# Performance work log

Measured on AMD Instinct MI355X. Metric: run time of the kernel, lower is better.

Reference implementation:

```python
import jax, jax.numpy as jnp
import numpy as np

B, S, EMB, HID, IMG, ATT, K, HL = 64, 512, 768, 512, 2048, 512, 6, 20


def setup_inputs() -> dict:
    key = jax.random.key(0)
    ks = jax.random.split(key, 14)
    u = lambda k, shape: jax.random.uniform(k, shape, jnp.float32, -0.1, 0.1)
    return {
        "representations": jax.random.normal(ks[0], (B, S, EMB), jnp.float32),
        "lengths": jax.random.randint(ks[1], (B,), 0, S),
        "separate_images": jax.random.normal(ks[2], (B, K, IMG), jnp.float32),
        "visual_context": jax.random.normal(ks[3], (B, K * IMG), jnp.float32),
        "prev_hist": jax.random.normal(ks[4], (B, K, HL, EMB), jnp.float32),
        "hist_counts": jax.random.randint(ks[5], (B, K), 0, HL + 1),
        "masks": jax.random.randint(ks[6], (B, S, 1), 0, 2).astype(bool),
        "W_sep": u(ks[7], (IMG, HID)), "b_sep": jnp.zeros((HID,), jnp.float32),
        "W_e2h": u(ks[8], (EMB, HID)), "b_e2h": jnp.zeros((HID,), jnp.float32),
        "W_hist": u(ks[9], (EMB, HID)), "b_hist": jnp.zeros((HID,), jnp.float32),
        "W_ctx": u(ks[10], (K * IMG, HID)), "b_ctx": jnp.zeros((HID,), jnp.float32),
        "W_mm": u(ks[11], (2 * HID, HID)), "b_mm": jnp.zeros((HID,), jnp.float32),
        "W_a1": u(ks[12], (HID, ATT)), "b_a1": jnp.zeros((ATT,), jnp.float32),
        "W_a2": u(ks[13], (ATT, 1)), "b_a2": jnp.zeros((1,), jnp.float32),
    }


def reference(representations, lengths, separate_images, visual_context,
              prev_hist, hist_counts, masks,
              W_sep, b_sep, W_e2h, b_e2h, W_hist, b_hist, W_ctx, b_ctx,
              W_mm, b_mm, W_a1, b_a1, W_a2, b_a2):
    # dropout_prob = 0 -> dropout is identity (eval-mode equivalence)
    input_reps = jax.nn.relu(representations @ W_e2h + b_e2h)          # [B,S,H]
    ctx = jax.nn.relu(visual_context @ W_ctx + b_ctx)                  # [B,H]
    ctx_rep = jnp.broadcast_to(ctx[:, None, :], input_reps.shape)
    mm = jax.nn.relu(jnp.concatenate([input_reps, ctx_rep], -1) @ W_mm + b_mm)  # [B,S,H]
    scores = jnp.tanh(mm @ W_a1 + b_a1) @ W_a2 + b_a2                  # [B,S,1]
    scores = jnp.where(masks, -jnp.inf, scores)
    att_w = jax.nn.softmax(scores, axis=1)                             # softmax over seq
    attended = jnp.sum(mm * att_w, axis=1)                             # [B,H]

    sep = separate_images @ W_sep + b_sep                              # [B,K,H]
    hl = prev_hist.shape[2]
    valid = jnp.arange(hl)[None, None, :] < hist_counts[:, :, None]    # [B,K,HL]
    hsum = jnp.sum(prev_hist * valid[..., None].astype(prev_hist.dtype), axis=2)
    havg = hsum / jnp.maximum(hist_counts, 1)[..., None].astype(prev_hist.dtype)
    hproj = jax.nn.relu(havg @ W_hist + b_hist)                        # [B,K,H]
    sep = sep + jnp.where((hist_counts > 0)[..., None], hproj, 0.0)
    sep = jax.nn.relu(sep)
    # F.normalize(p=2, dim=2, eps=1e-12)
    sep = sep / jnp.maximum(jnp.linalg.norm(sep, axis=2, keepdims=True), 1e-12)
    dot = jnp.einsum('bkh,bh->bk', sep, attended)[..., None]           # [B,K,1]
    return dot
```

## Files before the change

kernel.cpp:

```cpp
#include <hip/hip_runtime.h>
#include <math.h>

#define B_    64
#define S_    512
#define EMB_  768
#define HID_  512
#define IMG_  2048
#define ATT_  512
#define K_    6
#define HL_   20
#define MS_   (B_ * S_)

typedef __attribute__((ext_vector_type(8))) short bf16x8;
typedef __attribute__((ext_vector_type(4))) float f32x4;

__device__ __forceinline__ unsigned short f2b(float f) {
    unsigned int u = __float_as_uint(f);
    u += 0x7fffu + ((u >> 16) & 1u);
    return (unsigned short)(u >> 16);
}
__device__ __forceinline__ unsigned int pk_bf16(float lo, float hi) {
    unsigned int r;
    asm volatile("v_cvt_pk_bf16_f32 %0, %1, %2" : "=v"(r) : "v"(lo), "v"(hi));
    return r;
}

#define GLD_LDS16(gp, lp)                                                        \
    __builtin_amdgcn_global_load_lds(                                            \
        (const __attribute__((address_space(1))) void*)(gp),                     \
        (__attribute__((address_space(3))) void*)(lp), 16, 0, 0)

__global__ __launch_bounds__(256)
void prep(const float* __restrict__ W_e2h, const float* __restrict__ W_mm,
          const float* __restrict__ W_a1,
          unsigned short* __restrict__ WtE2H, unsigned short* __restrict__ WtMM,
          unsigned short* __restrict__ WtA1,
          const unsigned char* __restrict__ masks, int* __restrict__ flag) {
    const int z = blockIdx.z;
    if (z == 3) {
        if (blockIdx.x != 0 || blockIdx.y != 0) return;
        __shared__ int found;
        if (threadIdx.x == 0) found = 0;
        __syncthreads();
        for (int i = threadIdx.x; i < 8192; i += 256)
            if ((i & 3) != 0 && masks[i] != 0) found = 1;
        __syncthreads();
        if (threadIdx.x == 0) *flag = found;
        return;
    }
    const float* W;
    unsigned short* Wt;
    int Kd;
    if (z == 0)      { W = W_e2h; Wt = WtE2H; Kd = EMB_; }
    else if (z == 1) { W = W_mm;  Wt = WtMM;  Kd = HID_; }
    else             { W = W_a1;  Wt = WtA1;  Kd = HID_; }
    if ((int)blockIdx.x * 32 >= Kd) return;

    __shared__ float tile[32][33];
    int k0 = blockIdx.x * 32, n0 = blockIdx.y * 32;
    int tx = threadIdx.x & 31, ty = threadIdx.x >> 5;
    #pragma unroll
    for (int i = 0; i < 4; ++i)
        tile[ty + i * 8][tx] = W[(size_t)(k0 + ty + i * 8) * HID_ + n0 + tx];
    __syncthreads();
    #pragma unroll
    for (int i = 0; i < 4; ++i)
        Wt[(size_t)(n0 + ty + i * 8) * Kd + k0 + tx] = f2b(tile[tx][ty + i * 8]);
}

__device__ __forceinline__ void tile_coords(int N, int& bm, int& bn) {
    const int nwg = gridDim.x;
    const int cpx = nwg >> 3;
    const int lid = ((int)blockIdx.x & 7) * cpx + ((int)blockIdx.x >> 3);
    const int ntl = N >> 7;
    bn = (lid % ntl) << 7;
    bm = (lid / ntl) << 7;
}

template<bool AF32, int ACT, bool SCORE>
__global__ __launch_bounds__(256)
void gemm_bdir(const void* __restrict__ Av, const unsigned short* __restrict__ Bt,
               const float* __restrict__ bias, const float* __restrict__ row_add,
               int row_div, unsigned short* __restrict__ Co,
               const float* __restrict__ W_a2, float* __restrict__ scores8,
               int M, int N, int Kd) {
    __shared__ unsigned short Als[2][128 * 64];
    const int tid = threadIdx.x;
    int bm, bn; tile_coords(N, bm, bn);
    const int lane = tid & 63, wid = tid >> 6;
    const int wr = wid >> 1, wc = wid & 1;
    const int fr = lane & 15, hi = lane >> 4;

    const unsigned short* Ab = (const unsigned short*)Av;
    const float* Af = (const float*)Av;

    f32x4 acc[4][4] = {};

    int srow[4], lcol[4], scol[4];
    #pragma unroll
    for (int c = 0; c < 4; ++c) {
        int g = c * 256 + tid;
        srow[c] = g >> 3;
        lcol[c] = g & 7;
        scol[c] = lcol[c] ^ (srow[c] & 7);
    }

    const unsigned short* pB[4];
    #pragma unroll
    for (int n = 0; n < 4; ++n)
        pB[n] = Bt + (size_t)(bn + wc * 64 + n * 16 + fr) * Kd + hi * 8;

    float4 ra[8];

    auto stageA_lds = [&](int t, int buf) {
        #pragma unroll
        for (int c = 0; c < 4; ++c) {
            int g = c * 256 + tid;
            GLD_LDS16(Ab + (size_t)(bm + srow[c]) * Kd + t * 64 + scol[c] * 8,
                      &Als[buf][g * 8]);
        }
    };
    auto loadA = [&](int t) {
        #pragma unroll
        for (int c = 0; c < 4; ++c) {
            const float* p = Af + (size_t)(bm + srow[c]) * Kd + t * 64 + scol[c] * 8;
            ra[2 * c]     = *(const float4*)p;
            ra[2 * c + 1] = *(const float4*)(p + 4);
        }
    };
    auto writeA = [&](int buf) {
        #pragma unroll
        for (int c = 0; c < 4; ++c) {
            int g = c * 256 + tid;
            uint4 u;
            u.x = pk_bf16(ra[2*c].x,   ra[2*c].y);
            u.y = pk_bf16(ra[2*c].z,   ra[2*c].w);
            u.z = pk_bf16(ra[2*c+1].x, ra[2*c+1].y);
            u.w = pk_bf16(ra[2*c+1].z, ra[2*c+1].w);
            *(uint4*)&Als[buf][g * 8] = u;
        }
    };
    auto compute = [&](int buf, int t) {
        #pragma unroll
        for (int kk = 0; kk < 2; ++kk) {
            bf16x8 af[4], bv[4];
            #pragma unroll
            for (int n = 0; n < 4; ++n)
                bv[n] = *(const bf16x8*)(pB[n] + t * 64 + kk * 32);
            #pragma unroll
            for (int m = 0; m < 4; ++m) {
                int r = wr * 64 + m * 16 + fr;
                int sc = (kk * 4 + hi) ^ (fr & 7);
                af[m] = *(const bf16x8*)&Als[buf][r * 64 + sc * 8];
            }
            #pragma unroll
            for (int m = 0; m < 4; ++m)
                #pragma unroll
                for (int n = 0; n < 4; ++n)
                    acc[m][n] = __builtin_amdgcn_mfma_f32_16x16x32_bf16(af[m], bv[n], acc[m][n], 0, 0, 0);
        }
    };

    const int nt = Kd >> 6;

    if constexpr (AF32) {
        loadA(0);
        writeA(0);
    } else {
        stageA_lds(0, 0);
    }
    __syncthreads();

    for (int t = 0; t < nt; ++t) {
        const int buf = t & 1;
        const bool pf = (t + 1 < nt);
        if (pf) {
            if constexpr (AF32) loadA(t + 1);
            else                stageA_lds(t + 1, buf ^ 1);
        }
        compute(buf, t);
        if constexpr (AF32) {
            if (pf) writeA(buf ^ 1);
        }
        __syncthreads();
    }

    if (SCORE) {
        float ba[4], wa[4];
        #pragma unroll
        for (int n = 0; n < 4; ++n) {
            int col = bn + wc * 64 + n * 16 + fr;
            ba[n] = bias[col];
            wa[n] = W_a2[col];
        }
        const int slot = (bn >> 7) * 2 + wc;
        #pragma unroll
        for (int m = 0; m < 4; ++m) {
            #pragma unroll
            for (int r = 0; r < 4; ++r) {
                float p = 0.f;
                #pragma unroll
                for (int n = 0; n < 4; ++n)
                    p += tanhf(acc[m][n][r] + ba[n]) * wa[n];
                p += __shfl_xor(p, 1, 64);
                p += __shfl_xor(p, 2, 64);
                p += __shfl_xor(p, 4, 64);
                p += __shfl_xor(p, 8, 64);
                if (fr == 0)
                    scores8[(size_t)slot * M + bm + wr * 64 + m * 16 + hi * 4 + r] = p;
            }
        }
    } else {
        #pragma unroll
        for (int m = 0; m < 4; ++m) {
            #pragma unroll
            for (int n = 0; n < 4; ++n) {
                int col = bn + wc * 64 + n * 16 + fr;
                float badd = bias ? bias[col] : 0.f;
                #pragma unroll
                for (int r = 0; r < 4; ++r) {
                    int row = bm + wr * 64 + m * 16 + hi * 4 + r;
                    float x = acc[m][n][r] + badd;
                    if (row_add) x += row_add[(size_t)(row / row_div) * N + col];
                    if (ACT == 1) x = fmaxf(x, 0.f);
                    Co[(size_t)row * N + col] = f2b(x);
                }
            }
        }
    }
}

__global__ __launch_bounds__(256)
void gemm_splitk(const float* __restrict__ A, const float* __restrict__ W,
                 float* __restrict__ P, int M, int N, int Kd, int kps) {
    __shared__ float As[16][68];
    __shared__ float Ws[16][64];
    const int tid = threadIdx.x;
    const int bm = blockIdx.y * 64, bn = blockIdx.x * 64;
    const int ks = blockIdx.z;
    const int tx = tid & 15, ty = tid >> 4;
    const int arow = tid >> 2, akq = tid & 3;
    const int wk = tid >> 4, wnq = tid & 15;

    float acc[4][4] = {};
    const int kbeg = ks * kps, kend = kbeg + kps;

    for (int k0 = kbeg; k0 < kend; k0 += 16) {
        float4 av = *(const float4*)&A[(size_t)(bm + arow) * Kd + k0 + akq * 4];
        float4 wv = *(const float4*)&W[(size_t)(k0 + wk) * N + bn + wnq * 4];
        As[akq * 4 + 0][arow] = av.x;
        As[akq * 4 + 1][arow] = av.y;
        As[akq * 4 + 2][arow] = av.z;
        As[akq * 4 + 3][arow] = av.w;
        *(float4*)&Ws[wk][wnq * 4] = wv;
        __syncthreads();
        #pragma unroll
        for (int kk = 0; kk < 16; ++kk) {
            float4 a4 = *(const float4*)&As[kk][ty * 4];
            float4 b4 = *(const float4*)&Ws[kk][tx * 4];
            float a_[4] = {a4.x, a4.y, a4.z, a4.w};
            float b_[4] = {b4.x, b4.y, b4.z, b4.w};
            #pragma unroll
            for (int i = 0; i < 4; ++i)
                #pragma unroll
                for (int j = 0; j < 4; ++j)
                    acc[i][j] += a_[i] * b_[j];
        }
        __syncthreads();
    }

    float* Pbase = P + (size_t)ks * M * N;
    #pragma unroll
    for (int i = 0; i < 4; ++i) {
        int row = bm + ty * 4 + i;
        float4 v = {acc[i][0], acc[i][1], acc[i][2], acc[i][3]};
        *(float4*)&Pbase[(size_t)row * N + bn + tx * 4] = v;
    }
}

template<int ACT>
__global__ __launch_bounds__(256)
void reduce_k(const float* __restrict__ P, const float* __restrict__ bias,
              float* __restrict__ C, int MN, int N, int nsplit) {
    int idx = blockIdx.x * 256 + threadIdx.x;
    if (idx >= MN) return;
    float s = 0.f;
    for (int z = 0; z < nsplit; ++z) s += P[(size_t)z * MN + idx];
    if (bias) s += bias[idx & (N - 1)];
    if (ACT == 1) s = fmaxf(s, 0.f);
    C[idx] = s;
}

__global__ __launch_bounds__(256)
void softmax8(const float* __restrict__ scores8, const float* __restrict__ b_a2,
              const void* __restrict__ masks_raw, const int* __restrict__ flag,
              float* __restrict__ attw) {
    int b = blockIdx.x, tid = threadIdx.x;
    bool isb = (*flag) != 0;
    const unsigned char* mb = (const unsigned char*)masks_raw;
    const int* mi = (const int*)masks_raw;
    int lane = tid & 63, wv = tid >> 6;
    __shared__ float red[4], red2[4];
    float bias = b_a2[0];

    float m = -INFINITY;
    for (int s = tid; s < S_; s += 256) {
        int idx = b * S_ + s;
        float v = bias;
        #pragma unroll
        for (int z = 0; z < 8; ++z) v += scores8[(size_t)z * MS_ + idx];
        bool mk = isb ? (mb[idx] != 0) : (mi[idx] != 0);
        v = mk ? -INFINITY : v;
        attw[idx] = v;
        m = fmaxf(m, v);
    }
    #pragma unroll
    for (int off = 32; off; off >>= 1) m = fmaxf(m, __shfl_down(m, off, 64));
    if (lane == 0) red[wv] = m;
    __syncthreads();
    if (tid == 0) red[0] = fmaxf(fmaxf(red[0], red[1]), fmaxf(red[2], red[3]));
    __syncthreads();
    float Mx = red[0];

    float sum = 0.f;
    for (int s = tid; s < S_; s += 256) {
        int idx = b * S_ + s;
        float e = expf(attw[idx] - Mx);
        attw[idx] = e;
        sum += e;
    }
    #pragma unroll
    for (int off = 32; off; off >>= 1) sum += __shfl_down(sum, off, 64);
    if (lane == 0) red2[wv] = sum;
    __syncthreads();
    if (tid == 0) red2[0] = red2[0] + red2[1] + red2[2] + red2[3];
    __syncthreads();
    float inv = 1.f / red2[0];
    for (int s = tid; s < S_; s += 256) attw[b * S_ + s] *= inv;
}

__global__ __launch_bounds__(256)
void attended4(const unsigned short* __restrict__ mm, const float* __restrict__ attw,
               float* __restrict__ att4) {
    int b = blockIdx.x, z = blockIdx.y;
    int h2 = threadIdx.x;
    __shared__ float w[128];
    int s0 = z * 128;
    if (threadIdx.x < 128) w[threadIdx.x] = attw[b * S_ + s0 + threadIdx.x];
    __syncthreads();
    const unsigned int* base =
        (const unsigned int*)mm + ((size_t)b * S_ + s0) * (HID_ / 2) + h2;
    float a0 = 0.f, a1 = 0.f;
    for (int s = 0; s < 128; ++s) {
        unsigned int u = base[(size_t)s * (HID_ / 2)];
        a0 += __uint_as_float(u << 16) * w[s];
        a1 += __uint_as_float(u & 0xffff0000u) * w[s];
    }
    float2 r = {a0, a1};
    *(float2*)&att4[((size_t)z * B_ + b) * HID_ + h2 * 2] = r;
}

__global__ __launch_bounds__(256)
void hist_avg(const float* __restrict__ ph, const int* __restrict__ hcnt,
              float* __restrict__ havg) {
    int bk = blockIdx.x;
    int cnt = hcnt[bk];
    float denom = (float)(cnt > 1 ? cnt : 1);
    const float* base = ph + (size_t)bk * HL_ * EMB_;
    for (int e = threadIdx.x; e < EMB_; e += 256) {
        float s = 0.f;
        for (int l = 0; l < cnt; ++l) s += base[l * EMB_ + e];
        havg[bk * EMB_ + e] = s / denom;
    }
}

__global__ __launch_bounds__(256)
void combine_all(const float* __restrict__ skA, const float* __restrict__ skB,
                 const float* __restrict__ b_hist, const float* __restrict__ b_sep,
                 const int* __restrict__ hcnt, const float* __restrict__ att4,
                 float* __restrict__ out) {
    const int MNA = B_ * K_ * HID_;
    int bk = blockIdx.x, tid = threadIdx.x;
    int b = bk / K_;
    int cnt = hcnt[bk];
    float sq = 0.f, dt = 0.f;
    #pragma unroll
    for (int i = 0; i < HID_ / 256; ++i) {
        int h = tid + i * 256;
        size_t idx = (size_t)bk * HID_ + h;
        float hp = b_hist[h];
        #pragma unroll
        for (int z = 0; z < 8; ++z) hp += skA[(size_t)z * MNA + idx];
        hp = fmaxf(hp, 0.f);
        float sp = b_sep[h];
        #pragma unroll
        for (int z = 0; z < 16; ++z) sp += skB[(size_t)z * MNA + idx];
        float v = sp + (cnt > 0 ? hp : 0.f);
        v = fmaxf(v, 0.f);
        float at = 0.f;
        #pragma unroll
        for (int z = 0; z < 4; ++z) at += att4[((size_t)z * B_ + b) * HID_ + h];
        sq += v * v;
        dt += v * at;
    }
    #pragma unroll
    for (int off = 32; off; off >>= 1) {
        sq += __shfl_down(sq, off, 64);
        dt += __shfl_down(dt, off, 64);
    }
    __shared__ float rs[4], rd[4];
    int lane = tid & 63, wv = tid >> 6;
    if (lane == 0) { rs[wv] = sq; rd[wv] = dt; }
    __syncthreads();
    if (tid == 0) {
        float Sq = rs[0] + rs[1] + rs[2] + rs[3];
        float Dt = rd[0] + rd[1] + rd[2] + rd[3];
        float norm = fmaxf(sqrtf(Sq), 1e-12f);
        out[bk] = Dt / norm;
    }
}

extern "C" void kernel_launch(void* const* d_in, const int* in_sizes, int n_in,
                              void* d_out, int out_size, void* d_ws, size_t ws_size,
                              hipStream_t stream) {
    const float* reps     = (const float*)d_in[0];
    const float* sep_imgs = (const float*)d_in[2];
    const float* vctx     = (const float*)d_in[3];
    const float* phist    = (const float*)d_in[4];
    const int*   hcnt     = (const int*)d_in[5];
    const void*  masks    = d_in[6];
    const float* W_sep = (const float*)d_in[7];
    const float* b_sep = (const float*)d_in[8];
    const float* W_e2h = (const float*)d_in[9];
    const float* b_e2h = (const float*)d_in[10];
    const float* W_hist = (const float*)d_in[11];
    const float* b_hist = (const float*)d_in[12];
    const float* W_ctx = (const float*)d_in[13];
    const float* b_ctx = (const float*)d_in[14];
    const float* W_mm = (const float*)d_in[15];
    const float* b_mm = (const float*)d_in[16];
    const float* W_a1 = (const float*)d_in[17];
    const float* b_a1 = (const float*)d_in[18];
    const float* W_a2 = (const float*)d_in[19];
    const float* b_a2 = (const float*)d_in[20];
    float* out = (float*)d_out;

    const size_t MS = (size_t)MS_;
    const int MNA = B_ * K_ * HID_;

    unsigned short* actA  = (unsigned short*)d_ws;
    unsigned short* actB  = actA + MS * HID_;
    unsigned short* WtE2H = actB + MS * HID_;
    unsigned short* WtMM  = WtE2H + (size_t)EMB_ * HID_;
    unsigned short* WtA1  = WtMM + (size_t)HID_ * HID_;
    float* skC    = (float*)(WtA1 + (size_t)HID_ * HID_);
    float* skA    = skC + (size_t)64 * B_ * HID_;
    float* skB    = skA + (size_t)8 * MNA;
    float* scores8 = skB + (size_t)16 * MNA;
    float* attw   = scores8 + 8 * MS;
    float* att4   = attw + MS;
    float* ctx    = att4 + (size_t)4 * B_ * HID_;
    float* ctx2   = ctx + B_ * HID_;
    float* havg   = ctx2 + B_ * HID_;
    int*   flag   = (int*)(havg + (size_t)B_ * K_ * EMB_);

    prep<<<dim3(EMB_ / 32, HID_ / 32, 4), 256, 0, stream>>>(
        W_e2h, W_mm, W_a1, WtE2H, WtMM, WtA1, (const unsigned char*)masks, flag);

    {
        const int nsp = 64, kps = (K_ * IMG_) / nsp;
        gemm_splitk<<<dim3(8, 1, nsp), 256, 0, stream>>>(vctx, W_ctx, skC,
                                                         B_, HID_, K_ * IMG_, kps);
        reduce_k<1><<<(B_ * HID_ + 255) / 256, 256, 0, stream>>>(skC, b_ctx, ctx,
                                                                 B_ * HID_, HID_, nsp);
    }
    {
        const int nsp = 8, kps = HID_ / nsp;
        gemm_splitk<<<dim3(8, 1, nsp), 256, 0, stream>>>(ctx, W_mm + (size_t)HID_ * HID_,
                                                         skC, B_, HID_, HID_, kps);
        reduce_k<0><<<(B_ * HID_ + 255) / 256, 256, 0, stream>>>(skC, b_mm, ctx2,
                                                                 B_ * HID_, HID_, nsp);
    }

    const int big_grid = (MS_ / 128) * (HID_ / 128);
    gemm_bdir<true, 1, false><<<big_grid, 256, 0, stream>>>(
        reps, WtE2H, b_e2h, nullptr, 1, actA, nullptr, nullptr, MS_, HID_, EMB_);
    gemm_bdir<false, 1, false><<<big_grid, 256, 0, stream>>>(
        actA, WtMM, nullptr, ctx2, S_, actB, nullptr, nullptr, MS_, HID_, HID_);
    gemm_bdir<false, 0, true><<<big_grid, 256, 0, stream>>>(
        actB, WtA1, b_a1, nullptr, 1, actA, W_a2, scores8, MS_, ATT_, HID_);
    softmax8<<<B_, 256, 0, stream>>>(scores8, b_a2, masks, flag, attw);
    attended4<<<dim3(B_, 4), 256, 0, stream>>>(actB, attw, att4);
    hist_avg<<<B_ * K_, 256, 0, stream>>>(phist, hcnt, havg);
    gemm_splitk<<<dim3(8, 6, 8), 256, 0, stream>>>(havg, W_hist, skA,
                                                   B_ * K_, HID_, EMB_, EMB_ / 8);
    gemm_splitk<<<dim3(8, 6, 16), 256, 0, stream>>>(sep_imgs, W_sep, skB,
                                                    B_ * K_, HID_, IMG_, IMG_ / 16);
    combine_all<<<B_ * K_, 256, 0, stream>>>(skA, skB, b_hist, b_sep, hcnt,
                                             att4, out);
}
```

Measured before the change: 317.6 us.

## Stage B tiles through LDS with BK=32 and fuse softmax with attended sum

The big bf16 GEMMs now stage the B (weight) tile into LDS through direct global-to-LDS loads alongside A, instead of each wave reading B fragments straight from global memory, and the K-step shrinks from 64 to 32. This is meant to cut redundant global/L2 traffic for B and keep LDS usage about the same. The softmax and attention-weighted sum are also merged into one kernel that keeps the weights in shared memory, removing one launch and a global round-trip. The cost is that each batch now uses a single block of 256 threads to scan all 512 rows, giving less parallelism than the old 4-way split, and the smaller K-step doubles the number of barriers.

```diff
diff --git a/kernel.cpp b/kernel.cpp
--- a/kernel.cpp
+++ b/kernel.cpp
@@ -79,12 +79,13 @@
 
 template<bool AF32, int ACT, bool SCORE>
 __global__ __launch_bounds__(256)
-void gemm_bdir(const void* __restrict__ Av, const unsigned short* __restrict__ Bt,
-               const float* __restrict__ bias, const float* __restrict__ row_add,
-               int row_div, unsigned short* __restrict__ Co,
-               const float* __restrict__ W_a2, float* __restrict__ scores8,
-               int M, int N, int Kd) {
-    __shared__ unsigned short Als[2][128 * 64];
+void gemm_b32(const void* __restrict__ Av, const unsigned short* __restrict__ Bt,
+              const float* __restrict__ bias, const float* __restrict__ row_add,
+              int row_div, unsigned short* __restrict__ Co,
+              const float* __restrict__ W_a2, float* __restrict__ scores8,
+              int M, int N, int Kd) {
+    __shared__ unsigned short Als[2][128 * 32];
+    __shared__ unsigned short Bls[2][128 * 32];
     const int tid = threadIdx.x;
     int bm, bn; tile_coords(N, bm, bn);
     const int lane = tid & 63, wid = tid >> 6;
@@ -96,41 +97,43 @@
 
     f32x4 acc[4][4] = {};
 
-    int srow[4], lcol[4], scol[4];
-    #pragma unroll
-    for (int c = 0; c < 4; ++c) {
+    int srow[2], scol[2];
+    #pragma unroll
+    for (int c = 0; c < 2; ++c) {
         int g = c * 256 + tid;
-        srow[c] = g >> 3;
-        lcol[c] = g & 7;
-        scol[c] = lcol[c] ^ (srow[c] & 7);
-    }
-
-    const unsigned short* pB[4];
-    #pragma unroll
-    for (int n = 0; n < 4; ++n)
-        pB[n] = Bt + (size_t)(bn + wc * 64 + n * 16 + fr) * Kd + hi * 8;
-
-    float4 ra[8];
+        srow[c] = g >> 2;
+        scol[c] = (g & 3) ^ (srow[c] & 3);
+    }
+
+    float4 ra[4];
 
     auto stageA_lds = [&](int t, int buf) {
         #pragma unroll
-        for (int c = 0; c < 4; ++c) {
+        for (int c = 0; c < 2; ++c) {
             int g = c * 256 + tid;
-            GLD_LDS16(Ab + (size_t)(bm + srow[c]) * Kd + t * 64 + scol[c] * 8,
+            GLD_LDS16(Ab + (size_t)(bm + srow[c]) * Kd + t * 32 + scol[c] * 8,
                       &Als[buf][g * 8]);
+        }
+    };
+    auto stageB_lds = [&](int t, int buf) {
+        #pragma unroll
+        for (int c = 0; c < 2; ++c) {
+            int g = c * 256 + tid;
+            GLD_LDS16(Bt + (size_t)(bn + srow[c]) * Kd + t * 32 + scol[c] * 8,
+                      &Bls[buf][g * 8]);
         }
     };
     auto loadA = [&](int t) {
         #pragma unroll
-        for (int c = 0; c < 4; ++c) {
-            const float* p = Af + (size_t)(bm + srow[c]) * Kd + t * 64 + scol[c] * 8;
+        for (int c = 0; c < 2; ++c) {
+            const float* p = Af + (size_t)(bm + srow[c]) * Kd + t * 32 + scol[c] * 8;
             ra[2 * c]     = *(const float4*)p;
             ra[2 * c + 1] = *(const float4*)(p + 4);
         }
     };
     auto writeA = [&](int buf) {
         #pragma unroll
-        for (int c = 0; c < 4; ++c) {
+        for (int c = 0; c < 2; ++c) {
             int g = c * 256 + tid;
             uint4 u;
             u.x = pk_bf16(ra[2*c].x,   ra[2*c].y);
@@ -140,34 +143,34 @@
             *(uint4*)&Als[buf][g * 8] = u;
         }
     };
-    auto compute = [&](int buf, int t) {
-        #pragma unroll
-        for (int kk = 0; kk < 2; ++kk) {
-            bf16x8 af[4], bv[4];
+    auto compute = [&](int buf) {
+        bf16x8 af[4], bv[4];
+        #pragma unroll
+        for (int m = 0; m < 4; ++m) {
+            int r = wr * 64 + m * 16 + fr;
+            af[m] = *(const bf16x8*)&Als[buf][r * 32 + (hi ^ (r & 3)) * 8];
+        }
+        #pragma unroll
+        for (int n = 0; n < 4; ++n) {
+            int r = wc * 64 + n * 16 + fr;
+            bv[n] = *(const bf16x8*)&Bls[buf][r * 32 + (hi ^ (r & 3)) * 8];
+        }
+        #pragma unroll
+        for (int m = 0; m < 4; ++m)
             #pragma unroll
             for (int n = 0; n < 4; ++n)
-                bv[n] = *(const bf16x8*)(pB[n] + t * 64 + kk * 32);
-            #pragma unroll
-            for (int m = 0; m < 4; ++m) {
-                int r = wr * 64 + m * 16 + fr;
-                int sc = (kk * 4 + hi) ^ (fr & 7);
-                af[m] = *(const bf16x8*)&Als[buf][r * 64 + sc * 8];
-            }
-            #pragma unroll
-            for (int m = 0; m < 4; ++m)
-                #pragma unroll
-                for (int n = 0; n < 4; ++n)
-                    acc[m][n] = __builtin_amdgcn_mfma_f32_16x16x32_bf16(af[m], bv[n], acc[m][n], 0, 0, 0);
-        }
+                acc[m][n] = __builtin_amdgcn_mfma_f32_16x16x32_bf16(af[m], bv[n], acc[m][n], 0, 0, 0);
     };
 
-    const int nt = Kd >> 6;
+    const int nt = Kd >> 5;
 
     if constexpr (AF32) {
         loadA(0);
+        stageB_lds(0, 0);
         writeA(0);
     } else {
         stageA_lds(0, 0);
+        stageB_lds(0, 0);
     }
     __syncthreads();
 
@@ -175,10 +178,15 @@
         const int buf = t & 1;
         const bool pf = (t + 1 < nt);
         if (pf) {
-            if constexpr (AF32) loadA(t + 1);
-            else                stageA_lds(t + 1, buf ^ 1);
-        }
-        compute(buf, t);
+            if constexpr (AF32) {
+                loadA(t + 1);
+                stageB_lds(t + 1, buf ^ 1);
+            } else {
+                stageA_lds(t + 1, buf ^ 1);
+                stageB_lds(t + 1, buf ^ 1);
+            }
+        }
+        compute(buf);
         if constexpr (AF32) {
             if (pf) writeA(buf ^ 1);
         }
@@ -292,14 +300,15 @@
 }
 
 __global__ __launch_bounds__(256)
-void softmax8(const float* __restrict__ scores8, const float* __restrict__ b_a2,
-              const void* __restrict__ masks_raw, const int* __restrict__ flag,
-              float* __restrict__ attw) {
+void softmax_attended(const float* __restrict__ scores8, const float* __restrict__ b_a2,
+                      const void* __restrict__ masks_raw, const int* __restrict__ flag,
+                      const unsigned short* __restrict__ mm, float* __restrict__ att) {
     int b = blockIdx.x, tid = threadIdx.x;
     bool isb = (*flag) != 0;
     const unsigned char* mb = (const unsigned char*)masks_raw;
     const int* mi = (const int*)masks_raw;
     int lane = tid & 63, wv = tid >> 6;
+    __shared__ float w[S_];
     __shared__ float red[4], red2[4];
     float bias = b_a2[0];
 
@@ -311,7 +320,7 @@
         for (int z = 0; z < 8; ++z) v += scores8[(size_t)z * MS_ + idx];
         bool mk = isb ? (mb[idx] != 0) : (mi[idx] != 0);
         v = mk ? -INFINITY : v;
-        attw[idx] = v;
+        w[s] = v;
         m = fmaxf(m, v);
     }
     #pragma unroll
@@ -324,9 +333,8 @@
 
     float sum = 0.f;
     for (int s = tid; s < S_; s += 256) {
-        int idx = b * S_ + s;
-        float e = expf(attw[idx] - Mx);
-        attw[idx] = e;
+        float e = expf(w[s] - Mx);
+        w[s] = e;
         sum += e;
     }
     #pragma unroll
@@ -336,28 +344,20 @@
     if (tid == 0) red2[0] = red2[0] + red2[1] + red2[2] + red2[3];
     __syncthreads();
     float inv = 1.f / red2[0];
-    for (int s = tid; s < S_; s += 256) attw[b * S_ + s] *= inv;
-}
-
-__global__ __launch_bounds__(256)
-void attended4(const unsigned short* __restrict__ mm, const float* __restrict__ attw,
-               float* __restrict__ att4) {
-    int b = blockIdx.x, z = blockIdx.y;
-    int h2 = threadIdx.x;
-    __shared__ float w[128];
-    int s0 = z * 128;
-    if (threadIdx.x < 128) w[threadIdx.x] = attw[b * S_ + s0 + threadIdx.x];
-    __syncthreads();
+    for (int s = tid; s < S_; s += 256) w[s] *= inv;
+    __syncthreads();
+
     const unsigned int* base =
-        (const unsigned int*)mm + ((size_t)b * S_ + s0) * (HID_ / 2) + h2;
+        (const unsigned int*)mm + (size_t)b * S_ * (HID_ / 2) + tid;
     float a0 = 0.f, a1 = 0.f;
-    for (int s = 0; s < 128; ++s) {
+    #pragma unroll 4
+    for (int s = 0; s < S_; ++s) {
         unsigned int u = base[(size_t)s * (HID_ / 2)];
         a0 += __uint_as_float(u << 16) * w[s];
         a1 += __uint_as_float(u & 0xffff0000u) * w[s];
     }
     float2 r = {a0, a1};
-    *(float2*)&att4[((size_t)z * B_ + b) * HID_ + h2 * 2] = r;
+    *(float2*)&att[(size_t)b * HID_ + tid * 2] = r;
 }
 
 __global__ __launch_bounds__(256)
@@ -377,7 +377,7 @@
 __global__ __launch_bounds__(256)
 void combine_all(const float* __restrict__ skA, const float* __restrict__ skB,
                  const float* __restrict__ b_hist, const float* __restrict__ b_sep,
-                 const int* __restrict__ hcnt, const float* __restrict__ att4,
+                 const int* __restrict__ hcnt, const float* __restrict__ att,
                  float* __restrict__ out) {
     const int MNA = B_ * K_ * HID_;
     int bk = blockIdx.x, tid = threadIdx.x;
@@ -397,9 +397,7 @@
         for (int z = 0; z < 16; ++z) sp += skB[(size_t)z * MNA + idx];
         float v = sp + (cnt > 0 ? hp : 0.f);
         v = fmaxf(v, 0.f);
-        float at = 0.f;
-        #pragma unroll
-        for (int z = 0; z < 4; ++z) at += att4[((size_t)z * B_ + b) * HID_ + h];
+        float at = att[(size_t)b * HID_ + h];
         sq += v * v;
         dt += v * at;
     }
@@ -457,9 +455,8 @@
     float* skA    = skC + (size_t)64 * B_ * HID_;
     float* skB    = skA + (size_t)8 * MNA;
     float* scores8 = skB + (size_t)16 * MNA;
-    float* attw   = scores8 + 8 * MS;
-    float* att4   = attw + MS;
-    float* ctx    = att4 + (size_t)4 * B_ * HID_;
+    float* att    = scores8 + 8 * MS;
+    float* ctx    = att + (size_t)B_ * HID_;
     float* ctx2   = ctx + B_ * HID_;
     float* havg   = ctx2 + B_ * HID_;
     int*   flag   = (int*)(havg + (size_t)B_ * K_ * EMB_);
@@ -483,19 +480,18 @@
     }
 
     const int big_grid = (MS_ / 128) * (HID_ / 128);
-    gemm_bdir<true, 1, false><<<big_grid, 256, 0, stream>>>(
+    gemm_b32<true, 1, false><<<big_grid, 256, 0, stream>>>(
         reps, WtE2H, b_e2h, nullptr, 1, actA, nullptr, nullptr, MS_, HID_, EMB_);
-    gemm_bdir<false, 1, false><<<big_grid, 256, 0, stream>>>(
+    gemm_b32<false, 1, false><<<big_grid, 256, 0, stream>>>(
         actA, WtMM, nullptr, ctx2, S_, actB, nullptr, nullptr, MS_, HID_, HID_);
-    gemm_bdir<false, 0, true><<<big_grid, 256, 0, stream>>>(
+    gemm_b32<false, 0, true><<<big_grid, 256, 0, stream>>>(
         actB, WtA1, b_a1, nullptr, 1, actA, W_a2, scores8, MS_, ATT_, HID_);
-    softmax8<<<B_, 256, 0, stream>>>(scores8, b_a2, masks, flag, attw);
-    attended4<<<dim3(B_, 4), 256, 0, stream>>>(actB, attw, att4);
+    softmax_attended<<<B_, 256, 0, stream>>>(scores8, b_a2, masks, flag, actB, att);
     hist_avg<<<B_ * K_, 256, 0, stream>>>(phist, hcnt, havg);
     gemm_splitk<<<dim3(8, 6, 8), 256, 0, stream>>>(havg, W_hist, skA,
                                                    B_ * K_, HID_, EMB_, EMB_ / 8);
     gemm_splitk<<<dim3(8, 6, 16), 256, 0, stream>>>(sep_imgs, W_sep, skB,
                                                     B_ * K_, HID_, IMG_, IMG_ / 16);
     combine_all<<<B_ * K_, 256, 0, stream>>>(skA, skB, b_hist, b_sep, hcnt,
-                                             att4, out);
-}
+                                             att, out);
+}
```

New measurement: 312.0 us. No clear change (-1.8%).
